# Kernel optimization log

Hardware: AMD Instinct MI355X
Metric: run time of the kernel (lower is better)

The kernel has to match this reference:

```python
import jax, jax.numpy as jnp
import numpy as np

NEG_SLOPE = 0.2  # PyG GATConv leaky_relu slope


def _seg_sum(x, seg, n):
    return jax.ops.segment_sum(x, seg, num_segments=n)


def _seg_softmax(e, seg, n):
    # numerically stable softmax over edges grouped by destination node
    m = jax.ops.segment_max(e, seg, num_segments=n)
    w = jnp.exp(e - m[seg])
    s = jax.ops.segment_sum(w, seg, num_segments=n)
    return w / (s[seg] + 1e-16)


def _gat_bipartite(x_src, x_dst, Ws, Wd, a_s, a_d, b, src, dst, H=4, C=32):
    # PyG GATConv((x_src, x_dst), edge_index), concat=True, add_self_loops=False
    n_dst = x_dst.shape[0]
    hs = (x_src @ Ws).reshape(-1, H, C)   # [Ns,H,C]
    hd = (x_dst @ Wd).reshape(-1, H, C)   # [Nd,H,C]
    es = jnp.einsum('nhc,hc->nh', hs, a_s)  # alpha_src per node
    ed = jnp.einsum('nhc,hc->nh', hd, a_d)  # alpha_dst per node
    e = jax.nn.leaky_relu(es[src] + ed[dst], NEG_SLOPE)  # [E,H]
    alpha = _seg_softmax(e, dst, n_dst)                   # softmax per dst
    out = _seg_sum(hs[src] * alpha[..., None], dst, n_dst)  # [Nd,H,C]
    return out.reshape(n_dst, H * C) + b


def _gcn_self_loops(x, W, b, src, dst):
    # PyG GCNConv with add_self_loops=True, symmetric normalization
    n = x.shape[0]
    xw = x @ W
    deg = _seg_sum(jnp.ones_like(dst, dtype=xw.dtype), dst, n) + 1.0  # +1 self loop
    dinv = jax.lax.rsqrt(deg)
    coef = (dinv[src] * dinv[dst])[:, None]
    agg = _seg_sum(xw[src] * coef, dst, n)
    agg = agg + xw * (dinv * dinv)[:, None]  # self-loop contribution
    return agg + b


def setup_inputs() -> dict:
    D, H, C = 128, 4, 32
    Nb, Nc, Nt = 200_000, 20_000, 2_000
    Eadj, Ebc, Ect = 1_600_000, 200_000, 20_000
    key = jax.random.key(0)
    ks = jax.random.split(key, 24)
    g = 1.0 / np.sqrt(D)
    ga = 1.0 / np.sqrt(C)
    inp = {
        'x_building': jax.random.normal(ks[0], (Nb, D), jnp.float32),
        'x_cable': jax.random.normal(ks[1], (Nc, D), jnp.float32),
        'x_transformer': jax.random.normal(ks[2], (Nt, D), jnp.float32),
        'Ws1': jax.random.normal(ks[3], (D, D), jnp.float32) * g,
        'Wd1': jax.random.normal(ks[4], (D, D), jnp.float32) * g,
        'a_s1': jax.random.normal(ks[5], (H, C), jnp.float32) * ga,
        'a_d1': jax.random.normal(ks[6], (H, C), jnp.float32) * ga,
        'b1': jnp.zeros((D,), jnp.float32),
        'Ws2': jax.random.normal(ks[7], (D, D), jnp.float32) * g,
        'Wd2': jax.random.normal(ks[8], (D, D), jnp.float32) * g,
        'a_s2': jax.random.normal(ks[9], (H, C), jnp.float32) * ga,
        'a_d2': jax.random.normal(ks[10], (H, C), jnp.float32) * ga,
        'b2': jnp.zeros((D,), jnp.float32),
        'Wg': jax.random.normal(ks[11], (D, D), jnp.float32) * g,
        'bg': jnp.zeros((D,), jnp.float32),
        'b2c_src': jax.random.randint(ks[12], (Ebc,), 0, Nb, jnp.int32),
        'b2c_dst': jax.random.randint(ks[13], (Ebc,), 0, Nc, jnp.int32),
        'c2t_src': jax.random.randint(ks[14], (Ect,), 0, Nc, jnp.int32),
        'c2t_dst': jax.random.randint(ks[15], (Ect,), 0, Nt, jnp.int32),
        'adj_src': jax.random.randint(ks[16], (Eadj,), 0, Nb, jnp.int32),
        'adj_dst': jax.random.randint(ks[17], (Eadj,), 0, Nb, jnp.int32),
    }
    return inp


def reference(x_building, x_cable, x_transformer,
              Ws1, Wd1, a_s1, a_d1, b1,
              Ws2, Wd2, a_s2, a_d2, b2,
              Wg, bg,
              b2c_src, b2c_dst, c2t_src, c2t_dst, adj_src, adj_dst):
    # building -> cable_group (GAT), residual 0.5
    h_lv = _gat_bipartite(x_building, x_cable, Ws1, Wd1, a_s1, a_d1, b1,
                          b2c_src, b2c_dst)
    h_cable = x_cable + 0.5 * h_lv
    # (updated) cable_group -> transformer (GAT), residual 0.5
    h_tr = _gat_bipartite(h_cable, x_transformer, Ws2, Wd2, a_s2, a_d2, b2,
                          c2t_src, c2t_dst)
    h_transformer = x_transformer + 0.5 * h_tr
    # building adjacency (GCN with self loops), residual 0.2
    h_adj = _gcn_self_loops(x_building, Wg, bg, adj_src, adj_dst)
    h_building = x_building + 0.2 * h_adj
    return (h_building, h_cable, h_transformer)
```

## Files before the change

kernel.cpp:

```cpp
#include <hip/hip_runtime.h>
#include <hip/hip_bf16.h>
#include <stdint.h>

typedef __attribute__((ext_vector_type(8))) short bf16x8;
typedef __attribute__((ext_vector_type(4))) float floatx4;
typedef __attribute__((ext_vector_type(4))) float f32x4;
typedef __attribute__((ext_vector_type(2))) float f32x2;

__device__ __forceinline__ float2 bf2f(uint32_t u) {
  float2 r;
  r.x = __uint_as_float(u << 16);
  r.y = __uint_as_float(u & 0xffff0000u);
  return r;
}
__device__ __forceinline__ uint16_t f2bf(float f) {
  uint32_t u = __float_as_uint(f);
  uint32_t r = (u + 0x7fffu + ((u >> 16) & 1u)) >> 16;
  return (uint16_t)r;
}
__device__ __forceinline__ uint32_t f2bf_pack(float a, float b) {
  return (uint32_t)f2bf(a) | ((uint32_t)f2bf(b) << 16);
}
__device__ __forceinline__ int iclamp(int v, int lo, int hi) {
  return v < lo ? lo : (v > hi ? hi : v);
}
__device__ __forceinline__ float lrelu(float v) { return v >= 0.f ? v : 0.2f * v; }

__device__ __forceinline__ int detect_f32(const uint32_t* __restrict__ det) {
  uint32_t v = det[threadIdx.x & 63];
  int e = (v >> 23) & 0xFF;
  unsigned long long b = __ballot(e >= 90 && e <= 160);
  return __popcll(b) >= 48;
}

__device__ __forceinline__ void acc8(float* a, uint4 r, float w) {
  float2 f0 = bf2f(r.x), f1 = bf2f(r.y), f2 = bf2f(r.z), f3 = bf2f(r.w);
  a[0] += w * f0.x; a[1] += w * f0.y;
  a[2] += w * f1.x; a[3] += w * f1.y;
  a[4] += w * f2.x; a[5] += w * f2.y;
  a[6] += w * f3.x; a[7] += w * f3.y;
}

__global__ void transp_zero(const void* __restrict__ W0, const void* __restrict__ W1,
                            const void* __restrict__ W2, const void* __restrict__ W3,
                            const void* __restrict__ W4, __hip_bfloat16* __restrict__ WT,
                            int* __restrict__ zp, int zn, const uint32_t* __restrict__ det) {
  int isf32 = detect_f32(det);
  int b = blockIdx.x;
  int w = b >> 6;
  int i = (b & 63) * 256 + threadIdx.x;
  const void* W = (w == 0) ? W0 : (w == 1) ? W1 : (w == 2) ? W2 : (w == 3) ? W3 : W4;
  int k = i >> 7, n = i & 127;
  uint16_t h;
  if (isf32)
    h = f2bf(((const float*)W)[i]);
  else
    h = ((const uint16_t*)W)[i];
  ((uint16_t*)WT)[w * 16384 + n * 128 + k] = h;
  for (int j = blockIdx.x * 256 + threadIdx.x; j < zn; j += gridDim.x * 256) zp[j] = 0;
}

__global__ void hist_all(const int* __restrict__ d0, int E0, const int* __restrict__ d1,
                         int E1, const int* __restrict__ d2, int E2,
                         int* __restrict__ cnt, int n0, int n1, int n2) {
  int i = blockIdx.x * 256 + threadIdx.x;
  if (i < E0) {
    atomicAdd(&cnt[iclamp(d0[i], 0, n0 - 1)], 1);
  } else if (i < E0 + E1) {
    int j = i - E0;
    atomicAdd(&cnt[n0 + iclamp(d1[j], 0, n1 - 1)], 1);
  } else if (i < E0 + E1 + E2) {
    int j = i - E0 - E1;
    atomicAdd(&cnt[n0 + n1 + iclamp(d2[j], 0, n2 - 1)], 1);
  }
}

__global__ void scanp_all(const int* __restrict__ cnt, int* __restrict__ off,
                          int* __restrict__ bsum, int n0, int n1, int n2,
                          int nb0, int nb1) {
  int b = blockIdx.x;
  int seg, lb, base, n;
  if (b < nb0) { seg = 0; lb = b; base = 0; n = n0; }
  else if (b < nb0 + nb1) { seg = 1; lb = b - nb0; base = n0; n = n1; }
  else { seg = 2; lb = b - nb0 - nb1; base = n0 + n1; n = n2; }
  const int* in = cnt + base;
  int* out = off + base;
  int* bs = bsum + seg * 256;
  __shared__ int lds[256];
  int t = threadIdx.x;
  int pbase = lb * 1024 + t * 4;
  int v[4];
  int s = 0;
#pragma unroll
  for (int j = 0; j < 4; j++) {
    v[j] = (pbase + j < n) ? in[pbase + j] : 0;
    s += v[j];
  }
  lds[t] = s;
  __syncthreads();
  for (int d = 1; d < 256; d <<= 1) {
    int x = 0;
    if (t >= d) x = lds[t - d];
    __syncthreads();
    if (t >= d) lds[t] += x;
    __syncthreads();
  }
  int run = (t > 0) ? lds[t - 1] : 0;
  if (t == 255) bs[lb] = lds[255];
#pragma unroll
  for (int j = 0; j < 4; j++) {
    if (pbase + j < n) out[pbase + j] = run;
    run += v[j];
  }
}

__global__ void scans_all(int* __restrict__ bsum, int nb0, int nb1, int nb2) {
  int seg = blockIdx.x;
  int nb = (seg == 0) ? nb0 : (seg == 1) ? nb1 : nb2;
  int* bs = bsum + seg * 256;
  __shared__ int lds[256];
  int t = threadIdx.x;
  int v = (t < nb) ? bs[t] : 0;
  lds[t] = v;
  __syncthreads();
  for (int d = 1; d < 256; d <<= 1) {
    int x = 0;
    if (t >= d) x = lds[t - d];
    __syncthreads();
    if (t >= d) lds[t] += x;
    __syncthreads();
  }
  if (t < nb) bs[t] = (t > 0) ? lds[t - 1] : 0;
}

__global__ void scanadd_dinv(int* __restrict__ off, const int* __restrict__ bsum,
                             const int* __restrict__ cnt, float* __restrict__ dinv,
                             int n0, int n1, int n2) {
  int i = blockIdx.x * 256 + threadIdx.x;
  if (i >= n0 + n1 + n2) return;
  int seg, li;
  if (i < n0) { seg = 0; li = i; }
  else if (i < n0 + n1) { seg = 1; li = i - n0; }
  else { seg = 2; li = i - n0 - n1; }
  off[i] += bsum[seg * 256 + (li >> 10)];
  if (seg == 2) dinv[li] = rsqrtf((float)max(cnt[i], 0) + 1.0f);
}

struct MMB {
  const void *A0, *A1, *A2, *A3;
  unsigned long long ao0, ao1, ao2, ao3;
  const __hip_bfloat16 *W0, *W1, *W2, *W3;
  __hip_bfloat16 *O0, *O1, *O2, *O3;
  float *E0, *E1, *E2, *E3;
  const void *V0, *V1, *V2, *V3;
  int M0, M1, M2, M3;
  int B1, B2, B3;
};

struct FillJ {
  const int *s0, *d0, *s1, *d1, *s2, *d2;
  int E0, E1, E2;
  const int* off;
  int* cur;
  int *r0, *r1, *r2;
  int n0, n1, n2;
};

struct AggJob {
  const int* off; const int* cnt; const int* ssrc;
  const __hip_bfloat16* tab;
  const float* es; const float* ed;
  const float* dinv;
  const void* xdst; const void* bias;
  void* outb;
  unsigned long long ooff;
  int nt_out, N, Ns, E, isGcn;
};

__device__ __forceinline__ void mm_body(const MMB& p, int bid, int isf32) {
  const void* Abase;
  size_t aoff;
  const __hip_bfloat16* WTp;
  __hip_bfloat16* out;
  float* esp;
  const void* av;
  int M, bRow;
  if (bid >= p.B3) {
    Abase = p.A3; aoff = p.ao3; WTp = p.W3; out = p.O3; esp = p.E3; av = p.V3;
    M = p.M3; bRow = bid - p.B3;
  } else if (bid >= p.B2) {
    Abase = p.A2; aoff = p.ao2; WTp = p.W2; out = p.O2; esp = p.E2; av = p.V2;
    M = p.M2; bRow = bid - p.B2;
  } else if (bid >= p.B1) {
    Abase = p.A1; aoff = p.ao1; WTp = p.W1; out = p.O1; esp = p.E1; av = p.V1;
    M = p.M1; bRow = bid - p.B1;
  } else {
    Abase = p.A0; aoff = p.ao0; WTp = p.W0; out = p.O0; esp = p.E0; av = p.V0;
    M = p.M0; bRow = bid;
  }
  __shared__ __align__(16) __hip_bfloat16 w[128 * 136];
  int tid = threadIdx.x;
  for (int i = tid; i < 2048; i += 256) {
    int row = i >> 4, ch = i & 15;
    *(uint4*)&w[row * 136 + ch * 8] = *(const uint4*)&WTp[row * 128 + ch * 8];
  }
  __syncthreads();
  int wave = tid >> 6, lane = tid & 63;
  int l15 = lane & 15, kq = (lane >> 4) * 8;
  int row0 = bRow * 64 + wave * 16;
  int m = row0 + l15;
  int mc = m < M ? m : M - 1;
  floatx4 acc[8];
#pragma unroll
  for (int t = 0; t < 8; t++) acc[t] = (floatx4){0.f, 0.f, 0.f, 0.f};
#pragma unroll
  for (int k0 = 0; k0 < 128; k0 += 32) {
    union { bf16x8 v; uint32_t u[4]; } au;
    size_t eoff = aoff + (size_t)mc * 128 + k0 + kq;
    if (isf32) {
      const f32x4* Af = (const f32x4*)((const float*)Abase + eoff);
      f32x4 f0 = __builtin_nontemporal_load(Af);
      f32x4 f1 = __builtin_nontemporal_load(Af + 1);
      au.u[0] = f2bf_pack(f0.x, f0.y);
      au.u[1] = f2bf_pack(f0.z, f0.w);
      au.u[2] = f2bf_pack(f1.x, f1.y);
      au.u[3] = f2bf_pack(f1.z, f1.w);
    } else {
      au.v = __builtin_nontemporal_load((const bf16x8*)((const __hip_bfloat16*)Abase + eoff));
    }
#pragma unroll
    for (int t = 0; t < 8; t++) {
      bf16x8 b = *(const bf16x8*)&w[(t * 16 + l15) * 136 + k0 + kq];
      acc[t] = __builtin_amdgcn_mfma_f32_16x16x32_bf16(au.v, b, acc[t], 0, 0, 0);
    }
  }
  if (out) {
    int rbase = row0 + (lane >> 4) * 4;
    uint16_t* o16 = (uint16_t*)out;
#pragma unroll
    for (int r = 0; r < 4; r++) {
      int rr = rbase + r;
      if (rr < M) {
#pragma unroll
        for (int t = 0; t < 8; t++) o16[(size_t)rr * 128 + t * 16 + l15] = f2bf(acc[t][r]);
      }
    }
  }
  if (esp) {
    float av8[8];
    if (isf32) {
      const float* af = (const float*)av;
#pragma unroll
      for (int t = 0; t < 8; t++) av8[t] = af[t * 16 + l15];
    } else {
      const uint16_t* ab = (const uint16_t*)av;
#pragma unroll
      for (int t = 0; t < 8; t++) av8[t] = __uint_as_float((uint32_t)ab[t * 16 + l15] << 16);
    }
    float ph[4][4];
#pragma unroll
    for (int h = 0; h < 4; h++)
#pragma unroll
      for (int r = 0; r < 4; r++)
        ph[h][r] = acc[2 * h][r] * av8[2 * h] + acc[2 * h + 1][r] * av8[2 * h + 1];
#pragma unroll
    for (int h = 0; h < 4; h++)
#pragma unroll
      for (int r = 0; r < 4; r++) {
        float v = ph[h][r];
        v += __shfl_xor(v, 1);
        v += __shfl_xor(v, 2);
        v += __shfl_xor(v, 4);
        v += __shfl_xor(v, 8);
        ph[h][r] = v;
      }
    int rr = l15 >> 2, hh = l15 & 3;
    float s0 = (hh == 0) ? ph[0][0] : (hh == 1) ? ph[1][0] : (hh == 2) ? ph[2][0] : ph[3][0];
    float s1 = (hh == 0) ? ph[0][1] : (hh == 1) ? ph[1][1] : (hh == 2) ? ph[2][1] : ph[3][1];
    float s2 = (hh == 0) ? ph[0][2] : (hh == 1) ? ph[1][2] : (hh == 2) ? ph[2][2] : ph[3][2];
    float s3 = (hh == 0) ? ph[0][3] : (hh == 1) ? ph[1][3] : (hh == 2) ? ph[2][3] : ph[3][3];
    float val = (rr == 0) ? s0 : (rr == 1) ? s1 : (rr == 2) ? s2 : s3;
    int rowA = row0 + (lane >> 4) * 4 + rr;
    if (rowA < M) esp[(size_t)rowA * 4 + hh] = val;
  }
}

__device__ __forceinline__ void fill_body(const FillJ& f, int lb) {
  int i = lb * 256 + (int)threadIdx.x;
  const int* sp;
  const int* dp;
  int* rp;
  int base, N, E, j;
  if (i < f.E0) { sp = f.s0; dp = f.d0; rp = f.r0; base = 0; N = f.n0; E = f.E0; j = i; }
  else if (i < f.E0 + f.E1) { sp = f.s1; dp = f.d1; rp = f.r1; base = f.n0; N = f.n1; E = f.E1; j = i - f.E0; }
  else if (i < f.E0 + f.E1 + f.E2) { sp = f.s2; dp = f.d2; rp = f.r2; base = f.n0 + f.n1; N = f.n2; E = f.E2; j = i - f.E0 - f.E1; }
  else return;
  int d = iclamp(dp[j], 0, N - 1);
  int gi = base + d;
  int p = f.off[gi] + atomicAdd(&f.cur[gi], 1);
  rp[iclamp(p, 0, E - 1)] = sp[j];
}

__global__ __launch_bounds__(256) void mm_fill(MMB p, FillJ f, int Gmm,
                                               const uint32_t* __restrict__ det) {
  int isf32 = detect_f32(det);
  int bid = (int)blockIdx.x;
  if (bid < Gmm)
    mm_body(p, bid, isf32);
  else
    fill_body(f, bid - Gmm);
}

__device__ __forceinline__ void gat_body(const AggJob& j, int lb, int isf32) {
  int wid = (lb * 256 + (int)threadIdx.x) >> 6;
  if (wid >= j.N) return;
  int lane = threadIdx.x & 63;
  int g = lane >> 4, il = lane & 15;
  int hh = il >> 2;
  int c8 = il * 8;
  int deg = iclamp(j.cnt[wid], 0, j.E);
  int o = iclamp(j.off[wid], 0, j.E - deg);
  const int* sp = j.ssrc + o;
  float edv = j.ed[wid * 4 + hh];
  float a[8] = {0.f, 0.f, 0.f, 0.f, 0.f, 0.f, 0.f, 0.f};
  float wsum = 0.f;
  for (int e = 0; e < deg; e += 8) {
    int e0 = e + g, e1 = e0 + 4;
    if (e1 < deg) {
      int s0 = iclamp(sp[e0], 0, j.Ns - 1);
      int s1 = iclamp(sp[e1], 0, j.Ns - 1);
      uint4 r0 = *(const uint4*)&j.tab[(size_t)s0 * 128 + c8];
      uint4 r1 = *(const uint4*)&j.tab[(size_t)s1 * 128 + c8];
      float w0 = __expf(lrelu(j.es[s0 * 4 + hh] + edv));
      float w1 = __expf(lrelu(j.es[s1 * 4 + hh] + edv));
      wsum += w0 + w1;
      acc8(a, r0, w0);
      acc8(a, r1, w1);
    } else if (e0 < deg) {
      int s0 = iclamp(sp[e0], 0, j.Ns - 1);
      uint4 r0 = *(const uint4*)&j.tab[(size_t)s0 * 128 + c8];
      float w0 = __expf(lrelu(j.es[s0 * 4 + hh] + edv));
      wsum += w0;
      acc8(a, r0, w0);
    }
  }
#pragma unroll
  for (int q = 0; q < 8; q++) {
    a[q] += __shfl_xor(a[q], 16);
    a[q] += __shfl_xor(a[q], 32);
  }
  wsum += __shfl_xor(wsum, 16);
  wsum += __shfl_xor(wsum, 32);
  float inv = 1.f / (wsum + 1e-16f);
  int cc = c8 + g * 2;
  float v0, v1;
  if (g == 0)      { v0 = a[0]; v1 = a[1]; }
  else if (g == 1) { v0 = a[2]; v1 = a[3]; }
  else if (g == 2) { v0 = a[4]; v1 = a[5]; }
  else             { v0 = a[6]; v1 = a[7]; }
  v0 *= inv; v1 *= inv;
  float x0, x1, b0, b1;
  if (isf32) {
    const float* xf = (const float*)j.xdst + (size_t)wid * 128 + cc;
    x0 = xf[0]; x1 = xf[1];
    const float* bf_ = (const float*)j.bias + cc;
    b0 = bf_[0]; b1 = bf_[1];
  } else {
    float2 xf = bf2f(*(const uint32_t*)&((const __hip_bfloat16*)j.xdst)[(size_t)wid * 128 + cc]);
    float2 bv = bf2f(*(const uint32_t*)&((const __hip_bfloat16*)j.bias)[cc]);
    x0 = xf.x; x1 = xf.y; b0 = bv.x; b1 = bv.y;
  }
  float r0 = x0 + 0.5f * (v0 + b0);
  float r1 = x1 + 0.5f * (v1 + b1);
  if (isf32) {
    f32x2* op = (f32x2*)((float*)j.outb + j.ooff + (size_t)wid * 128 + cc);
    f32x2 rv = {r0, r1};
    if (j.nt_out) __builtin_nontemporal_store(rv, op);
    else *op = rv;
  } else {
    *(uint32_t*)&((uint16_t*)j.outb)[j.ooff + (size_t)wid * 128 + cc] = f2bf_pack(r0, r1);
  }
}

__device__ __forceinline__ void gcn_body(const AggJob& j, int lb, int isf32) {
  int wid = (lb * 256 + (int)threadIdx.x) >> 6;
  if (wid >= j.N) return;
  int lane = threadIdx.x & 63;
  int g = lane >> 4, il = lane & 15;
  int c8 = il * 8;
  int deg = iclamp(j.cnt[wid], 0, j.E);
  int o = iclamp(j.off[wid], 0, j.E - deg);
  const int* sp = j.ssrc + o;
  float di = j.dinv[wid];
  float a[8] = {0.f, 0.f, 0.f, 0.f, 0.f, 0.f, 0.f, 0.f};
  for (int e = 0; e < deg; e += 8) {
    int e0 = e + g, e1 = e0 + 4;
    if (e1 < deg) {
      int s0 = iclamp(sp[e0], 0, j.Ns - 1);
      int s1 = iclamp(sp[e1], 0, j.Ns - 1);
      uint4 r0 = *(const uint4*)&j.tab[(size_t)s0 * 128 + c8];
      uint4 r1 = *(const uint4*)&j.tab[(size_t)s1 * 128 + c8];
      float d0 = j.dinv[s0], d1 = j.dinv[s1];
      acc8(a, r0, d0);
      acc8(a, r1, d1);
    } else if (e0 < deg) {
      int s0 = iclamp(sp[e0], 0, j.Ns - 1);
      uint4 r0 = *(const uint4*)&j.tab[(size_t)s0 * 128 + c8];
      float d0 = j.dinv[s0];
      acc8(a, r0, d0);
    }
  }
  if (g == 0) {
    uint4 sr = *(const uint4*)&j.tab[(size_t)wid * 128 + c8];
    acc8(a, sr, di);
  }
#pragma unroll
  for (int q = 0; q < 8; q++) {
    a[q] += __shfl_xor(a[q], 16);
    a[q] += __shfl_xor(a[q], 32);
  }
  int cc = c8 + g * 2;
  float v0, v1;
  if (g == 0)      { v0 = a[0]; v1 = a[1]; }
  else if (g == 1) { v0 = a[2]; v1 = a[3]; }
  else if (g == 2) { v0 = a[4]; v1 = a[5]; }
  else             { v0 = a[6]; v1 = a[7]; }
  float agg0 = di * v0;
  float agg1 = di * v1;
  float x0, x1, b0, b1;
  if (isf32) {
    f32x2 xf = __builtin_nontemporal_load(
        (const f32x2*)((const float*)j.xdst + (size_t)wid * 128 + cc));
    x0 = xf.x; x1 = xf.y;
    const float* bf_ = (const float*)j.bias + cc;
    b0 = bf_[0]; b1 = bf_[1];
  } else {
    float2 xf = bf2f(*(const uint32_t*)&((const __hip_bfloat16*)j.xdst)[(size_t)wid * 128 + cc]);
    float2 bv = bf2f(*(const uint32_t*)&((const __hip_bfloat16*)j.bias)[cc]);
    x0 = xf.x; x1 = xf.y; b0 = bv.x; b1 = bv.y;
  }
  float r0 = x0 + 0.2f * (agg0 + b0);
  float r1 = x1 + 0.2f * (agg1 + b1);
  if (isf32) {
    f32x2 rv = {r0, r1};
    __builtin_nontemporal_store(rv, (f32x2*)((float*)j.outb + j.ooff + (size_t)wid * 128 + cc));
  } else {
    *(uint32_t*)&((uint16_t*)j.outb)[j.ooff + (size_t)wid * 128 + cc] = f2bf_pack(r0, r1);
  }
}

__global__ __launch_bounds__(256) void agg_pair(AggJob j0, AggJob j1, int G0,
                                                const uint32_t* __restrict__ det) {
  int isf32 = detect_f32(det);
  int bid = (int)blockIdx.x;
  if (bid < G0) {
    if (j0.isGcn) gcn_body(j0, bid, isf32);
    else gat_body(j0, bid, isf32);
  } else {
    int lb = bid - G0;
    if (j1.isGcn) gcn_body(j1, lb, isf32);
    else gat_body(j1, lb, isf32);
  }
}

extern "C" void kernel_launch(void* const* d_in, const int* in_sizes, int n_in,
                              void* d_out, int out_size, void* d_ws, size_t ws_size,
                              hipStream_t stream) {
  const void* xb = d_in[0];
  const void* xc = d_in[1];
  const void* xt = d_in[2];
  const void* Ws1 = d_in[3];
  const void* Wd1 = d_in[4];
  const void* a_s1 = d_in[5];
  const void* a_d1 = d_in[6];
  const void* b1 = d_in[7];
  const void* Ws2 = d_in[8];
  const void* Wd2 = d_in[9];
  const void* a_s2 = d_in[10];
  const void* a_d2 = d_in[11];
  const void* b2 = d_in[12];
  const void* Wg = d_in[13];
  const void* bg = d_in[14];
  const int* b2c_src = (const int*)d_in[15];
  const int* b2c_dst = (const int*)d_in[16];
  const int* c2t_src = (const int*)d_in[17];
  const int* c2t_dst = (const int*)d_in[18];
  const int* adj_src = (const int*)d_in[19];
  const int* adj_dst = (const int*)d_in[20];

  const int Nb = in_sizes[0] / 128, Nc = in_sizes[1] / 128, Nt = in_sizes[2] / 128;
  const int Ebc = in_sizes[15], Ect = in_sizes[17], Eadj = in_sizes[19];
  const int nAll = Nc + Nt + Nb;
  const int Eall = Ebc + Ect + Eadj;
  const int BIG = 0x7fffffff;

  auto al = [](size_t x) { return (x + 255) & ~(size_t)255; };
  char* base = (char*)d_ws;

  size_t o = 0;
  size_t o_WT = o;     o += al((size_t)5 * 16384 * 2);
  size_t o_cnt = o;    o += al((size_t)nAll * 4);
  size_t o_cur = o;    o += al((size_t)nAll * 4);
  size_t o_off = o;    o += al((size_t)nAll * 4);
  size_t o_dinv = o;   o += al((size_t)Nb * 4);
  size_t o_bsum = o;   o += al(3 * 256 * 4);
  size_t o_srtbc = o;  o += al((size_t)Ebc * 4);
  size_t o_srtct = o;  o += al((size_t)Ect * 4);
  size_t o_srtadj = o; o += al((size_t)Eadj * 4);
  size_t o_es1 = o;    o += al((size_t)Nb * 16);
  size_t o_ed1 = o;    o += al((size_t)Nc * 16);
  size_t o_es2 = o;    o += al((size_t)Nc * 16);
  size_t o_ed2 = o;    o += al((size_t)Nt * 16);
  size_t o_hs2 = o;    o += al((size_t)Nc * 256);
  size_t o_XW = o;     o += al((size_t)Nb * 256);
  size_t endB = o;
  size_t o_XWg = o;    o += al((size_t)Nb * 256);
  size_t endA = o;
  if (endB > ws_size) return;
  const bool pathA = (endA <= ws_size);

  const uint32_t* det = (const uint32_t*)Ws1;
  __hip_bfloat16* WT = (__hip_bfloat16*)(base + o_WT);
  int* cnt = (int*)(base + o_cnt);
  int* cur = (int*)(base + o_cur);
  int* off = (int*)(base + o_off);
  float* dinv = (float*)(base + o_dinv);
  int* bsum = (int*)(base + o_bsum);
  int* srt_bc = (int*)(base + o_srtbc);
  int* srt_ct = (int*)(base + o_srtct);
  int* srt_adj = (int*)(base + o_srtadj);
  float* es1 = (float*)(base + o_es1);
  float* ed1 = (float*)(base + o_ed1);
  float* es2 = (float*)(base + o_es2);
  float* ed2 = (float*)(base + o_ed2);
  __hip_bfloat16* hs2 = (__hip_bfloat16*)(base + o_hs2);
  __hip_bfloat16* XW = (__hip_bfloat16*)(base + o_XW);
  __hip_bfloat16* XWg = (__hip_bfloat16*)(base + o_XWg);

  const size_t off_b_out = 0;
  const size_t off_c_out = (size_t)Nb * 128;
  const size_t off_t_out = off_c_out + (size_t)Nc * 128;

  int* cnt_c = cnt;
  int* cnt_t = cnt + Nc;
  int* cnt_b = cnt + Nc + Nt;
  int* off_c = off;
  int* off_t = off + Nc;
  int* off_b = off + Nc + Nt;

  int zn = (int)((o_off - o_cnt) / 4);
  transp_zero<<<320, 256, 0, stream>>>(Ws1, Wd1, Ws2, Wd2, Wg, WT, cnt, zn, det);

  hist_all<<<(Eall + 255) / 256, 256, 0, stream>>>(b2c_dst, Ebc, c2t_dst, Ect, adj_dst,
                                                   Eadj, cnt, Nc, Nt, Nb);

  int nb0 = (Nc + 1023) / 1024, nb1 = (Nt + 1023) / 1024, nb2 = (Nb + 1023) / 1024;
  scanp_all<<<nb0 + nb1 + nb2, 256, 0, stream>>>(cnt, off, bsum, Nc, Nt, Nb, nb0, nb1);
  scans_all<<<3, 256, 0, stream>>>(bsum, nb0, nb1, nb2);
  scanadd_dinv<<<(nAll + 255) / 256, 256, 0, stream>>>(off, bsum, cnt, dinv, Nc, Nt, Nb);

  FillJ fj;
  fj.s0 = b2c_src; fj.d0 = b2c_dst; fj.s1 = c2t_src; fj.d1 = c2t_dst;
  fj.s2 = adj_src; fj.d2 = adj_dst;
  fj.E0 = Ebc; fj.E1 = Ect; fj.E2 = Eadj;
  fj.off = off; fj.cur = cur;
  fj.r0 = srt_bc; fj.r1 = srt_ct; fj.r2 = srt_adj;
  fj.n0 = Nc; fj.n1 = Nt; fj.n2 = Nb;
  int Gfill = (Eall + 255) / 256;

  int g0 = (Nb + 63) / 64, g1 = (Nc + 63) / 64, g2 = (Nt + 63) / 64;

  {
    MMB p;
    p.A0 = xb; p.ao0 = 0; p.W0 = WT + 0 * 16384; p.O0 = XW;      p.E0 = es1; p.V0 = a_s1; p.M0 = Nb;
    p.A1 = xc; p.ao1 = 0; p.W1 = WT + 1 * 16384; p.O1 = nullptr; p.E1 = ed1; p.V1 = a_d1; p.M1 = Nc;
    p.A2 = xt; p.ao2 = 0; p.W2 = WT + 3 * 16384; p.O2 = nullptr; p.E2 = ed2; p.V2 = a_d2; p.M2 = Nt;
    p.A3 = xb; p.ao3 = 0; p.W3 = WT + 4 * 16384; p.O3 = XWg;     p.E3 = nullptr; p.V3 = nullptr; p.M3 = Nb;
    p.B1 = g0; p.B2 = g0 + g1;
    p.B3 = pathA ? (g0 + g1 + g2) : BIG;
    int Gmm = g0 + g1 + g2 + (pathA ? g0 : 0);
    mm_fill<<<Gmm + Gfill, 256, 0, stream>>>(p, fj, Gmm, det);
  }

  AggJob ja1;
  ja1.off = off_c; ja1.cnt = cnt_c; ja1.ssrc = srt_bc; ja1.tab = XW;
  ja1.es = es1; ja1.ed = ed1; ja1.dinv = nullptr;
  ja1.xdst = xc; ja1.bias = b1; ja1.outb = d_out; ja1.ooff = off_c_out;
  ja1.nt_out = 0; ja1.N = Nc; ja1.Ns = Nb; ja1.E = Ebc; ja1.isGcn = 0;
  int Ga1 = (Nc + 3) / 4;

  AggJob jg;
  jg.off = off_b; jg.cnt = cnt_b; jg.ssrc = srt_adj;
  jg.tab = pathA ? XWg : XW;
  jg.es = nullptr; jg.ed = nullptr; jg.dinv = dinv;
  jg.xdst = xb; jg.bias = bg; jg.outb = d_out; jg.ooff = off_b_out;
  jg.nt_out = 1; jg.N = Nb; jg.Ns = Nb; jg.E = Eadj; jg.isGcn = 1;
  int Gg = (Nb + 3) / 4;

  AggJob ja2;
  ja2.off = off_t; ja2.cnt = cnt_t; ja2.ssrc = srt_ct; ja2.tab = hs2;
  ja2.es = es2; ja2.ed = ed2; ja2.dinv = nullptr;
  ja2.xdst = xt; ja2.bias = b2; ja2.outb = d_out; ja2.ooff = off_t_out;
  ja2.nt_out = 1; ja2.N = Nt; ja2.Ns = Nc; ja2.E = Ect; ja2.isGcn = 0;
  int Ga2 = (Nt + 3) / 4;

  if (pathA) {
    agg_pair<<<Gg + Ga1, 256, 0, stream>>>(jg, ja1, Gg, det);
    MMB p;
    p.A0 = d_out; p.ao0 = off_c_out; p.W0 = WT + 2 * 16384; p.O0 = hs2; p.E0 = es2; p.V0 = a_s2; p.M0 = Nc;
    p.A1 = nullptr; p.ao1 = 0; p.W1 = nullptr; p.O1 = nullptr; p.E1 = nullptr; p.V1 = nullptr; p.M1 = 0;
    p.A2 = nullptr; p.ao2 = 0; p.W2 = nullptr; p.O2 = nullptr; p.E2 = nullptr; p.V2 = nullptr; p.M2 = 0;
    p.A3 = nullptr; p.ao3 = 0; p.W3 = nullptr; p.O3 = nullptr; p.E3 = nullptr; p.V3 = nullptr; p.M3 = 0;
    p.B1 = BIG; p.B2 = BIG; p.B3 = BIG;
    mm_fill<<<g1, 256, 0, stream>>>(p, fj, g1, det);
    agg_pair<<<Ga2, 256, 0, stream>>>(ja2, ja2, Ga2, det);
  } else {
    agg_pair<<<Ga1, 256, 0, stream>>>(ja1, ja1, Ga1, det);
    MMB p;
    p.A0 = d_out; p.ao0 = off_c_out; p.W0 = WT + 2 * 16384; p.O0 = hs2; p.E0 = es2; p.V0 = a_s2; p.M0 = Nc;
    p.A1 = xb; p.ao1 = 0; p.W1 = WT + 4 * 16384; p.O1 = XW; p.E1 = nullptr; p.V1 = nullptr; p.M1 = Nb;
    p.A2 = nullptr; p.ao2 = 0; p.W2 = nullptr; p.O2 = nullptr; p.E2 = nullptr; p.V2 = nullptr; p.M2 = 0;
    p.A3 = nullptr; p.ao3 = 0; p.W3 = nullptr; p.O3 = nullptr; p.E3 = nullptr; p.V3 = nullptr; p.M3 = 0;
    p.B1 = g1; p.B2 = BIG; p.B3 = BIG;
    mm_fill<<<g1 + g0, 256, 0, stream>>>(p, fj, g1 + g0, det);
    agg_pair<<<Gg + Ga2, 256, 0, stream>>>(jg, ja2, Gg, det);
  }
}
```

Measured before the change: 609.8 us.

## Fuse dual building GEMMs per block and merge weight-transpose with histogram

```diff
diff --git a/kernel.cpp b/kernel.cpp
--- a/kernel.cpp
+++ b/kernel.cpp
@@ -41,37 +41,37 @@
   a[6] += w * f3.x; a[7] += w * f3.y;
 }
 
-__global__ void transp_zero(const void* __restrict__ W0, const void* __restrict__ W1,
-                            const void* __restrict__ W2, const void* __restrict__ W3,
-                            const void* __restrict__ W4, __hip_bfloat16* __restrict__ WT,
-                            int* __restrict__ zp, int zn, const uint32_t* __restrict__ det) {
-  int isf32 = detect_f32(det);
+__global__ void prep_k(const void* __restrict__ W0, const void* __restrict__ W1,
+                       const void* __restrict__ W2, const void* __restrict__ W3,
+                       const void* __restrict__ W4, __hip_bfloat16* __restrict__ WT,
+                       const int* __restrict__ d0, int E0, const int* __restrict__ d1,
+                       int E1, const int* __restrict__ d2, int E2,
+                       int* __restrict__ cnt, int n0, int n1, int n2,
+                       const uint32_t* __restrict__ det) {
   int b = blockIdx.x;
-  int w = b >> 6;
-  int i = (b & 63) * 256 + threadIdx.x;
-  const void* W = (w == 0) ? W0 : (w == 1) ? W1 : (w == 2) ? W2 : (w == 3) ? W3 : W4;
-  int k = i >> 7, n = i & 127;
-  uint16_t h;
-  if (isf32)
-    h = f2bf(((const float*)W)[i]);
-  else
-    h = ((const uint16_t*)W)[i];
-  ((uint16_t*)WT)[w * 16384 + n * 128 + k] = h;
-  for (int j = blockIdx.x * 256 + threadIdx.x; j < zn; j += gridDim.x * 256) zp[j] = 0;
-}
-
-__global__ void hist_all(const int* __restrict__ d0, int E0, const int* __restrict__ d1,
-                         int E1, const int* __restrict__ d2, int E2,
-                         int* __restrict__ cnt, int n0, int n1, int n2) {
-  int i = blockIdx.x * 256 + threadIdx.x;
-  if (i < E0) {
-    atomicAdd(&cnt[iclamp(d0[i], 0, n0 - 1)], 1);
-  } else if (i < E0 + E1) {
-    int j = i - E0;
-    atomicAdd(&cnt[n0 + iclamp(d1[j], 0, n1 - 1)], 1);
-  } else if (i < E0 + E1 + E2) {
-    int j = i - E0 - E1;
-    atomicAdd(&cnt[n0 + n1 + iclamp(d2[j], 0, n2 - 1)], 1);
+  if (b < 320) {
+    int isf32 = detect_f32(det);
+    int w = b >> 6;
+    int i = (b & 63) * 256 + threadIdx.x;
+    const void* W = (w == 0) ? W0 : (w == 1) ? W1 : (w == 2) ? W2 : (w == 3) ? W3 : W4;
+    int k = i >> 7, n = i & 127;
+    uint16_t h;
+    if (isf32)
+      h = f2bf(((const float*)W)[i]);
+    else
+      h = ((const uint16_t*)W)[i];
+    ((uint16_t*)WT)[w * 16384 + n * 128 + k] = h;
+  } else {
+    int i = (b - 320) * 256 + threadIdx.x;
+    if (i < E0) {
+      atomicAdd(&cnt[iclamp(d0[i], 0, n0 - 1)], 1);
+    } else if (i < E0 + E1) {
+      int j = i - E0;
+      atomicAdd(&cnt[n0 + iclamp(d1[j], 0, n1 - 1)], 1);
+    } else if (i < E0 + E1 + E2) {
+      int j = i - E0 - E1;
+      atomicAdd(&cnt[n0 + n1 + iclamp(d2[j], 0, n2 - 1)], 1);
+    }
   }
 }
 
@@ -155,6 +155,7 @@
   const void *V0, *V1, *V2, *V3;
   int M0, M1, M2, M3;
   int B1, B2, B3;
+  int dual;
 };
 
 struct FillJ {
@@ -198,6 +199,7 @@
     Abase = p.A0; aoff = p.ao0; WTp = p.W0; out = p.O0; esp = p.E0; av = p.V0;
     M = p.M0; bRow = bid;
   }
+  const bool dualThis = (p.dual != 0) && (bid < p.B1);
   __shared__ __align__(16) __hip_bfloat16 w[128 * 136];
   int tid = threadIdx.x;
   for (int i = tid; i < 2048; i += 256) {
@@ -219,14 +221,16 @@
     size_t eoff = aoff + (size_t)mc * 128 + k0 + kq;
     if (isf32) {
       const f32x4* Af = (const f32x4*)((const float*)Abase + eoff);
-      f32x4 f0 = __builtin_nontemporal_load(Af);
-      f32x4 f1 = __builtin_nontemporal_load(Af + 1);
+      f32x4 f0, f1;
+      if (dualThis) { f0 = Af[0]; f1 = Af[1]; }
+      else { f0 = __builtin_nontemporal_load(Af); f1 = __builtin_nontemporal_load(Af + 1); }
       au.u[0] = f2bf_pack(f0.x, f0.y);
       au.u[1] = f2bf_pack(f0.z, f0.w);
       au.u[2] = f2bf_pack(f1.x, f1.y);
       au.u[3] = f2bf_pack(f1.z, f1.w);
     } else {
-      au.v = __builtin_nontemporal_load((const bf16x8*)((const __hip_bfloat16*)Abase + eoff));
+      const bf16x8* Ab = (const bf16x8*)((const __hip_bfloat16*)Abase + eoff);
+      au.v = dualThis ? *Ab : __builtin_nontemporal_load(Ab);
     }
 #pragma unroll
     for (int t = 0; t < 8; t++) {
@@ -282,6 +286,51 @@
     float val = (rr == 0) ? s0 : (rr == 1) ? s1 : (rr == 2) ? s2 : s3;
     int rowA = row0 + (lane >> 4) * 4 + rr;
     if (rowA < M) esp[(size_t)rowA * 4 + hh] = val;
+  }
+  if (dualThis) {
+    __syncthreads();
+    for (int i = tid; i < 2048; i += 256) {
+      int row = i >> 4, ch = i & 15;
+      *(uint4*)&w[row * 136 + ch * 8] = *(const uint4*)&p.W3[row * 128 + ch * 8];
+    }
+    __syncthreads();
+    int mc2 = m < p.M3 ? m : p.M3 - 1;
+    floatx4 acc2[8];
+#pragma unroll
+    for (int t = 0; t < 8; t++) acc2[t] = (floatx4){0.f, 0.f, 0.f, 0.f};
+#pragma unroll
+    for (int k0 = 0; k0 < 128; k0 += 32) {
+      union { bf16x8 v; uint32_t u[4]; } au;
+      size_t eoff = p.ao0 + (size_t)mc2 * 128 + k0 + kq;
+      if (isf32) {
+        const f32x4* Af = (const f32x4*)((const float*)p.A0 + eoff);
+        f32x4 f0 = Af[0];
+        f32x4 f1 = Af[1];
+        au.u[0] = f2bf_pack(f0.x, f0.y);
+        au.u[1] = f2bf_pack(f0.z, f0.w);
+        au.u[2] = f2bf_pack(f1.x, f1.y);
+        au.u[3] = f2bf_pack(f1.z, f1.w);
+      } else {
+        au.v = *(const bf16x8*)((const __hip_bfloat16*)p.A0 + eoff);
+      }
+#pragma unroll
+      for (int t = 0; t < 8; t++) {
+        bf16x8 b = *(const bf16x8*)&w[(t * 16 + l15) * 136 + k0 + kq];
+        acc2[t] = __builtin_amdgcn_mfma_f32_16x16x32_bf16(au.v, b, acc2[t], 0, 0, 0);
+      }
+    }
+    if (p.O3) {
+      int rbase = row0 + (lane >> 4) * 4;
+      uint16_t* o16 = (uint16_t*)p.O3;
+#pragma unroll
+      for (int r = 0; r < 4; r++) {
+        int rr = rbase + r;
+        if (rr < p.M3) {
+#pragma unroll
+          for (int t = 0; t < 8; t++) o16[(size_t)rr * 128 + t * 16 + l15] = f2bf(acc2[t][r]);
+        }
+      }
+    }
   }
 }
 
@@ -361,8 +410,9 @@
   v0 *= inv; v1 *= inv;
   float x0, x1, b0, b1;
   if (isf32) {
-    const float* xf = (const float*)j.xdst + (size_t)wid * 128 + cc;
-    x0 = xf[0]; x1 = xf[1];
+    f32x2 xf = __builtin_nontemporal_load(
+        (const f32x2*)((const float*)j.xdst + (size_t)wid * 128 + cc));
+    x0 = xf.x; x1 = xf.y;
     const float* bf_ = (const float*)j.bias + cc;
     b0 = bf_[0]; b1 = bf_[1];
   } else {
@@ -548,11 +598,12 @@
   int* off_t = off + Nc;
   int* off_b = off + Nc + Nt;
 
-  int zn = (int)((o_off - o_cnt) / 4);
-  transp_zero<<<320, 256, 0, stream>>>(Ws1, Wd1, Ws2, Wd2, Wg, WT, cnt, zn, det);
-
-  hist_all<<<(Eall + 255) / 256, 256, 0, stream>>>(b2c_dst, Ebc, c2t_dst, Ect, adj_dst,
-                                                   Eadj, cnt, Nc, Nt, Nb);
+  hipMemsetAsync(base + o_cnt, 0, o_off - o_cnt, stream);
+
+  int Ghist = (Eall + 255) / 256;
+  prep_k<<<320 + Ghist, 256, 0, stream>>>(Ws1, Wd1, Ws2, Wd2, Wg, WT, b2c_dst, Ebc,
+                                          c2t_dst, Ect, adj_dst, Eadj, cnt, Nc, Nt, Nb,
+                                          det);
 
   int nb0 = (Nc + 1023) / 1024, nb1 = (Nt + 1023) / 1024, nb2 = (Nb + 1023) / 1024;
   scanp_all<<<nb0 + nb1 + nb2, 256, 0, stream>>>(cnt, off, bsum, Nc, Nt, Nb, nb0, nb1);
@@ -575,10 +626,11 @@
     p.A0 = xb; p.ao0 = 0; p.W0 = WT + 0 * 16384; p.O0 = XW;      p.E0 = es1; p.V0 = a_s1; p.M0 = Nb;
     p.A1 = xc; p.ao1 = 0; p.W1 = WT + 1 * 16384; p.O1 = nullptr; p.E1 = ed1; p.V1 = a_d1; p.M1 = Nc;
     p.A2 = xt; p.ao2 = 0; p.W2 = WT + 3 * 16384; p.O2 = nullptr; p.E2 = ed2; p.V2 = a_d2; p.M2 = Nt;
-    p.A3 = xb; p.ao3 = 0; p.W3 = WT + 4 * 16384; p.O3 = XWg;     p.E3 = nullptr; p.V3 = nullptr; p.M3 = Nb;
-    p.B1 = g0; p.B2 = g0 + g1;
-    p.B3 = pathA ? (g0 + g1 + g2) : BIG;
-    int Gmm = g0 + g1 + g2 + (pathA ? g0 : 0);
+    p.A3 = xb; p.ao3 = 0; p.W3 = WT + 4 * 16384; p.O3 = pathA ? XWg : nullptr;
+    p.E3 = nullptr; p.V3 = nullptr; p.M3 = Nb;
+    p.B1 = g0; p.B2 = g0 + g1; p.B3 = BIG;
+    p.dual = pathA ? 1 : 0;
+    int Gmm = g0 + g1 + g2;
     mm_fill<<<Gmm + Gfill, 256, 0, stream>>>(p, fj, Gmm, det);
   }
 
@@ -611,7 +663,7 @@
     p.A1 = nullptr; p.ao1 = 0; p.W1 = nullptr; p.O1 = nullptr; p.E1 = nullptr; p.V1 = nullptr; p.M1 = 0;
     p.A2 = nullptr; p.ao2 = 0; p.W2 = nullptr; p.O2 = nullptr; p.E2 = nullptr; p.V2 = nullptr; p.M2 = 0;
     p.A3 = nullptr; p.ao3 = 0; p.W3 = nullptr; p.O3 = nullptr; p.E3 = nullptr; p.V3 = nullptr; p.M3 = 0;
-    p.B1 = BIG; p.B2 = BIG; p.B3 = BIG;
+    p.B1 = BIG; p.B2 = BIG; p.B3 = BIG; p.dual = 0;
     mm_fill<<<g1, 256, 0, stream>>>(p, fj, g1, det);
     agg_pair<<<Ga2, 256, 0, stream>>>(ja2, ja2, Ga2, det);
   } else {
@@ -621,7 +673,7 @@
     p.A1 = xb; p.ao1 = 0; p.W1 = WT + 4 * 16384; p.O1 = XW; p.E1 = nullptr; p.V1 = nullptr; p.M1 = Nb;
     p.A2 = nullptr; p.ao2 = 0; p.W2 = nullptr; p.O2 = nullptr; p.E2 = nullptr; p.V2 = nullptr; p.M2 = 0;
     p.A3 = nullptr; p.ao3 = 0; p.W3 = nullptr; p.O3 = nullptr; p.E3 = nullptr; p.V3 = nullptr; p.M3 = 0;
-    p.B1 = g1; p.B2 = BIG; p.B3 = BIG;
+    p.B1 = g1; p.B2 = BIG; p.B3 = BIG; p.dual = 0;
     mm_fill<<<g1 + g0, 256, 0, stream>>>(p, fj, g1 + g0, det);
     agg_pair<<<Gg + Ga2, 256, 0, stream>>>(jg, ja2, Gg, det);
   }
```

Measured after the change: 567.2 us. 7.0% less time.
